# Kernel optimization log

Measured on AMD Instinct MI355X. Metric: run time of the kernel, lower is better.

## Reference

```python
import jax, jax.numpy as jnp
import numpy as np

HIDDEN = 2048
NUM_HEADS = 32
GROUP_SIZE = 4
HEAD_DIM = HIDDEN // NUM_HEADS            # 64
GROUP_NUM = NUM_HEADS // GROUP_SIZE       # 8 KV heads
B, S = 2, 2048


def setup_inputs() -> dict:
    key = jax.random.key(0)
    ks = jax.random.split(key, 7)
    sc = 1.0 / np.sqrt(HIDDEN)
    x = jax.random.normal(ks[0], (B, S, HIDDEN), dtype=jnp.float32)
    attention_mask = jnp.ones((B, S), dtype=jnp.int32)
    Wq = jax.random.normal(ks[1], (HIDDEN, HIDDEN), dtype=jnp.float32) * sc
    bq = jax.random.normal(ks[2], (HIDDEN,), dtype=jnp.float32) * 0.02
    Wk = jax.random.normal(ks[3], (HIDDEN, GROUP_NUM * HEAD_DIM), dtype=jnp.float32) * sc
    bk = jax.random.normal(ks[4], (GROUP_NUM * HEAD_DIM,), dtype=jnp.float32) * 0.02
    Wv = jax.random.normal(ks[5], (HIDDEN, GROUP_NUM * HEAD_DIM), dtype=jnp.float32) * sc
    bv = jax.random.normal(ks[6], (GROUP_NUM * HEAD_DIM,), dtype=jnp.float32) * 0.02
    return {"x": x, "attention_mask": attention_mask,
            "Wq": Wq, "bq": bq, "Wk": Wk, "bk": bk, "Wv": Wv, "bv": bv}


def reference(x, attention_mask, Wq, bq, Wk, bk, Wv, bv):
    b, s, _ = x.shape
    # projections
    q = (x @ Wq + bq).reshape(b, s, NUM_HEADS, HEAD_DIM).transpose(0, 2, 1, 3)   # (B,H,S,hd)
    k = (x @ Wk + bk).reshape(b, s, GROUP_NUM, HEAD_DIM).transpose(0, 2, 1, 3)   # (B,G,S,hd)
    v = (x @ Wv + bv).reshape(b, s, GROUP_NUM, HEAD_DIM).transpose(0, 2, 1, 3)
    # expand KV groups to full head count (head h uses group h // group_size)
    k = jnp.repeat(k, GROUP_SIZE, axis=1)                                        # (B,H,S,hd)
    v = jnp.repeat(v, GROUP_SIZE, axis=1)
    # NOTE: original torch code uses floor-division `//` for scaling and no softmax
    score = jnp.floor(jnp.einsum('bhqd,bhkd->bhqk', q, k) / np.sqrt(HEAD_DIM).astype(np.float32))
    score = jnp.where(attention_mask[:, None, None, :] == 0, -jnp.inf, score)
    out = jnp.einsum('bhqk,bhkd->bhqd', score, v)                                # (B,H,S,hd)
    return out.transpose(0, 2, 1, 3).reshape(b, s, HIDDEN)
```

## Files before the change

kernel.cpp:

```cpp
#include <hip/hip_runtime.h>
#include <math.h>

#define HIDDEN 2048
#define NHEADS 32
#define HDIM 64
#define GNUM 8
#define KVDIM 512
#define BB 2
#define SS 2048
#define MROWS (BB * SS)
#define NQKV 3072

typedef _Float16 half8 __attribute__((ext_vector_type(8)));
typedef _Float16 half4 __attribute__((ext_vector_type(4)));
typedef _Float16 half2 __attribute__((ext_vector_type(2)));
typedef __fp16 fp16x2 __attribute__((ext_vector_type(2)));
typedef float floatx4 __attribute__((ext_vector_type(4)));

#define MFMA16(a, b, c) __builtin_amdgcn_mfma_f32_16x16x32_f16((a), (b), (c), 0, 0, 0)

__device__ __forceinline__ void split_f32(float x, _Float16& hi, _Float16& lo) {
    hi = (_Float16)x;
    lo = (_Float16)((x - (float)hi) * 2048.0f);
}

__device__ __forceinline__ void load_lds16(const void* g, void* l) {
    __builtin_amdgcn_global_load_lds(
        (const __attribute__((address_space(1))) void*)g,
        (__attribute__((address_space(3))) void*)l, 16, 0, 0);
}

__device__ __forceinline__ void permswap32(unsigned& a, unsigned& b) {
    asm volatile("v_permlane32_swap_b32 %0, %1" : "+v"(a), "+v"(b));
}
__device__ __forceinline__ void permswap16(unsigned& a, unsigned& b) {
    asm volatile("v_permlane16_swap_b32 %0, %1" : "+v"(a), "+v"(b));
}

__device__ __forceinline__ unsigned pk_f16(float a, float b) {
    union { fp16x2 h; unsigned u; } c;
    c.h = __builtin_amdgcn_cvt_pkrtz(a, b);
    return c.u;
}

__global__ __launch_bounds__(256)
void split_x(const float* __restrict__ x, _Float16* __restrict__ xh,
             _Float16* __restrict__ xl, int n4) {
    for (int idx = blockIdx.x * 256 + threadIdx.x; idx < n4; idx += gridDim.x * 256) {
        floatx4 v = reinterpret_cast<const floatx4*>(x)[idx];
        half4 h, l;
        #pragma unroll
        for (int e = 0; e < 4; ++e) { _Float16 hi, lo; split_f32(v[e], hi, lo); h[e] = hi; l[e] = lo; }
        reinterpret_cast<half4*>(xh)[idx] = h;
        reinterpret_cast<half4*>(xl)[idx] = l;
    }
}

__global__ __launch_bounds__(256)
void split_wt(const float* __restrict__ W, int N, int n0,
              _Float16* __restrict__ Wth, _Float16* __restrict__ Wtl) {
    __shared__ float tile[64][68];
    const int tid = threadIdx.x;
    const int kb = blockIdx.x, nb = blockIdx.y;
    #pragma unroll
    for (int i = 0; i < 4; ++i) {
        int idx = tid + i * 256;
        int r = idx >> 4, c4 = idx & 15;
        floatx4 v = *reinterpret_cast<const floatx4*>(&W[(size_t)(kb * 64 + r) * N + nb * 64 + c4 * 4]);
        *reinterpret_cast<floatx4*>(&tile[r][c4 * 4]) = v;
    }
    __syncthreads();
    #pragma unroll
    for (int i = 0; i < 4; ++i) {
        int idx = tid + i * 256;
        int r2 = idx >> 4, c2 = (idx & 15) * 4;
        half4 h, l;
        #pragma unroll
        for (int e = 0; e < 4; ++e) {
            _Float16 hi, lo;
            split_f32(tile[c2 + e][r2], hi, lo);
            h[e] = hi; l[e] = lo;
        }
        size_t o = (size_t)(n0 + nb * 64 + r2) * HIDDEN + kb * 64 + c2;
        *reinterpret_cast<half4*>(&Wth[o]) = h;
        *reinterpret_cast<half4*>(&Wtl[o]) = l;
    }
}

__global__ __launch_bounds__(256)
void biascat_k(const float* __restrict__ bq, const float* __restrict__ bk,
               const float* __restrict__ bv, float* __restrict__ bias) {
    int i = blockIdx.x * 256 + threadIdx.x;
    if (i < 2048) bias[i] = bq[i];
    else if (i < 2560) bias[i] = bk[i - 2048];
    else if (i < NQKV) bias[i] = bv[i - 2560];
}

__global__ __launch_bounds__(256, 2)
void gemm_qkv(const _Float16* __restrict__ xh, const _Float16* __restrict__ xl,
              const _Float16* __restrict__ Wth, const _Float16* __restrict__ Wtl,
              const float* __restrict__ bias,
              _Float16* __restrict__ qh, _Float16* __restrict__ ql,
              _Float16* __restrict__ khs, _Float16* __restrict__ kls,
              _Float16* __restrict__ vh) {
    __shared__ __align__(16) _Float16 Ah[128 * 64];
    __shared__ __align__(16) _Float16 Al[128 * 64];
    __shared__ __align__(16) _Float16 Bh[128 * 64];
    __shared__ __align__(16) _Float16 Bl[128 * 64];

    const int tid  = threadIdx.x;
    const int lane = tid & 63;
    const int w    = tid >> 6;
    const int wm   = w >> 1, wn = w & 1;
    const int bm   = blockIdx.x, bn = blockIdx.y;
    const int ml   = lane & 15;
    const int kg8  = (lane >> 4) * 8;

    const _Float16* gsrc;
    _Float16* ldst;
    if      (w == 0) { gsrc = xh  + (size_t)(bm * 128) * HIDDEN; ldst = Ah; }
    else if (w == 1) { gsrc = xl  + (size_t)(bm * 128) * HIDDEN; ldst = Al; }
    else if (w == 2) { gsrc = Wth + (size_t)(bn * 128) * HIDDEN; ldst = Bh; }
    else             { gsrc = Wtl + (size_t)(bn * 128) * HIDDEN; ldst = Bl; }

    floatx4 acc0[4][4] = {};
    floatx4 accL[4][4] = {};

    for (int k0 = 0; k0 < HIDDEN; k0 += 64) {
        #pragma unroll
        for (int i = 0; i < 16; ++i) {
            int L   = i * 1024 + lane * 16;
            int row = L >> 7;
            int off = (L & 127) ^ ((row & 7) << 4);
            const void* gp = (const char*)(gsrc + (size_t)row * HIDDEN + k0) + off;
            void* lp = (char*)ldst + i * 1024;
            load_lds16(gp, lp);
        }
        __syncthreads();

        #pragma unroll
        for (int kc = 0; kc < 2; ++kc) {
            half8 a_h[4], a_l[4], b_h[4], b_l[4];
            #pragma unroll
            for (int r = 0; r < 4; ++r) {
                int row = wm * 64 + r * 16 + ml;
                int byt = row * 128 + (((kc * 64 + kg8 * 2)) ^ ((row & 7) << 4));
                a_h[r] = *reinterpret_cast<const half8*>((const char*)Ah + byt);
                a_l[r] = *reinterpret_cast<const half8*>((const char*)Al + byt);
            }
            #pragma unroll
            for (int c = 0; c < 4; ++c) {
                int row = wn * 64 + c * 16 + ml;
                int byt = row * 128 + (((kc * 64 + kg8 * 2)) ^ ((row & 7) << 4));
                b_h[c] = *reinterpret_cast<const half8*>((const char*)Bh + byt);
                b_l[c] = *reinterpret_cast<const half8*>((const char*)Bl + byt);
            }
            #pragma unroll
            for (int r = 0; r < 4; ++r)
                #pragma unroll
                for (int c = 0; c < 4; ++c) {
                    acc0[r][c] = MFMA16(a_h[r], b_h[c], acc0[r][c]);
                    accL[r][c] = MFMA16(a_h[r], b_l[c], accL[r][c]);
                    accL[r][c] = MFMA16(a_l[r], b_h[c], accL[r][c]);
                }
        }
        __syncthreads();
    }

    #pragma unroll
    for (int c = 0; c < 4; ++c) {
        int colg = bn * 128 + wn * 64 + c * 16 + ml;
        float bval = bias[colg];
        #pragma unroll
        for (int r = 0; r < 4; ++r) {
            int rowg = bm * 128 + wm * 64 + r * 16 + (lane >> 4) * 4;
            #pragma unroll
            for (int reg = 0; reg < 4; ++reg) {
                float val = acc0[r][c][reg] + accL[r][c][reg] * (1.0f / 2048.0f) + bval;
                int rr = rowg + reg;
                if (colg < 2048) {
                    _Float16 hi, lo; split_f32(val, hi, lo);
                    qh[(size_t)rr * HIDDEN + colg] = hi;
                    ql[(size_t)rr * HIDDEN + colg] = lo;
                } else if (colg < 2560) {
                    int ck = colg - 2048;
                    int gk = ck >> 6, dk = ck & 63;
                    int bk_ = rr >> 11, sk_ = rr & 2047;
                    int kk = sk_ & 63;
                    size_t baseK = ((size_t)((bk_ * 8 + gk) * 32 + (sk_ >> 6))) * 4096
                                 + kk * 64 + (dk ^ ((kk & 7) << 3));
                    _Float16 hi, lo; split_f32(val, hi, lo);
                    khs[baseK] = hi;
                    kls[baseK] = lo;
                } else {
                    vh[(size_t)rr * KVDIM + (colg - 2560)] = (_Float16)val;
                }
            }
        }
    }
}

__global__ __launch_bounds__(256, 2)
void attn5(const _Float16* __restrict__ qh, const _Float16* __restrict__ ql,
           const _Float16* __restrict__ khs, const _Float16* __restrict__ kls,
           const _Float16* __restrict__ vh, const int* __restrict__ mask,
           float* __restrict__ out) {
    __shared__ __align__(16) _Float16 Ksh[64 * 64];
    __shared__ __align__(16) _Float16 Ksl[64 * 64];
    __shared__ __align__(16) _Float16 Vst[64][72];

    const int tid  = threadIdx.x;
    const int lane = tid & 63;
    const int w    = tid >> 6;
    const int ml   = lane & 15;
    const int lg   = lane >> 4;
    const int kg8  = lg * 8;

    const int f_  = blockIdx.y * 32 + blockIdx.x;
    const int bg  = (f_ & 7) | ((f_ >> 8) << 3);
    const int qt  = (f_ >> 3) & 31;
    const int b   = bg >> 3, g = bg & 7;

    half8 qhf[4][2], qlf[4][2];
    {
        size_t rowbase = (size_t)(b * SS + qt * 64 + w * 16 + ml) * HIDDEN;
        #pragma unroll
        for (int hh = 0; hh < 4; ++hh) {
            int hcol = (g * 4 + hh) * HDIM;
            #pragma unroll
            for (int gch = 0; gch < 2; ++gch) {
                half8 a = *reinterpret_cast<const half8*>(&qh[rowbase + hcol + gch * 32 + kg8]);
                half8 c = *reinterpret_cast<const half8*>(&ql[rowbase + hcol + gch * 32 + kg8]);
                qhf[hh][gch] = a * (_Float16)0.125f;
                qlf[hh][gch] = c * (_Float16)0.125f;
            }
        }
    }

    const _Float16* ktile_h = khs + (size_t)(bg * 32) * 4096;
    const _Float16* ktile_l = kls + (size_t)(bg * 32) * 4096;
    const _Float16* vbg = vh + (size_t)b * SS * KVDIM + g * HDIM;
    const int* mb = mask + b * SS;

    floatx4 oacc[4][4] = {};

    for (int kt = 0; kt < SS / 64; ++kt) {
        __syncthreads();
        if (w == 0) {
            #pragma unroll
            for (int j = 0; j < 8; ++j)
                load_lds16((const char*)(ktile_h + (size_t)kt * 4096) + j * 1024 + lane * 16,
                           (char*)Ksh + j * 1024);
        } else if (w == 1) {
            #pragma unroll
            for (int j = 0; j < 8; ++j)
                load_lds16((const char*)(ktile_l + (size_t)kt * 4096) + j * 1024 + lane * 16,
                           (char*)Ksl + j * 1024);
        }
        {
            int rp = (tid & 31) * 2, c8 = (tid >> 5) * 8;
            half8 v0 = *reinterpret_cast<const half8*>(&vbg[(size_t)(kt * 64 + rp) * KVDIM + c8]);
            half8 v1 = *reinterpret_cast<const half8*>(&vbg[(size_t)(kt * 64 + rp + 1) * KVDIM + c8]);
            #pragma unroll
            for (int e = 0; e < 8; ++e)
                *reinterpret_cast<half2*>(&Vst[c8 + e][rp]) = half2{v0[e], v1[e]};
        }
        __syncthreads();

        half8 av[4][2];
        #pragma unroll
        for (int f = 0; f < 4; ++f)
            #pragma unroll
            for (int kc = 0; kc < 2; ++kc)
                av[f][kc] = *reinterpret_cast<const half8*>(&Vst[f * 16 + ml][kc * 32 + kg8]);

        int4 m4v[4];
        #pragma unroll
        for (int fc = 0; fc < 4; ++fc)
            m4v[fc] = *reinterpret_cast<const int4*>(&mb[kt * 64 + fc * 16 + lg * 4]);

        __builtin_amdgcn_s_setprio(1);

        unsigned h2[4][4][2];
        #pragma unroll
        for (int fc = 0; fc < 4; ++fc) {
            int krow = fc * 16 + ml;
            int xo = (krow & 7) << 3;
            half8 k_h[2], k_l[2];
            #pragma unroll
            for (int gch = 0; gch < 2; ++gch) {
                k_h[gch] = *reinterpret_cast<const half8*>(&Ksh[krow * 64 + ((gch * 32 + kg8) ^ xo)]);
                k_l[gch] = *reinterpret_cast<const half8*>(&Ksl[krow * 64 + ((gch * 32 + kg8) ^ xo)]);
            }
            #pragma unroll
            for (int hh = 0; hh < 4; ++hh) {
                floatx4 s0 = {}, sl = {};
                s0 = MFMA16(k_h[0], qhf[hh][0], s0);
                s0 = MFMA16(k_h[1], qhf[hh][1], s0);
                sl = MFMA16(k_l[0], qhf[hh][0], sl);
                sl = MFMA16(k_l[1], qhf[hh][1], sl);
                sl = MFMA16(k_h[0], qlf[hh][0], sl);
                sl = MFMA16(k_h[1], qlf[hh][1], sl);
                float sv[4];
                #pragma unroll
                for (int r = 0; r < 4; ++r) {
                    float t = floorf(fmaf(sl[r], 1.0f / 2048.0f, s0[r]));
                    sv[r] = (m4v[fc][r] == 0) ? -INFINITY : t;
                }
                h2[hh][fc][0] = pk_f16(sv[0], sv[1]);
                h2[hh][fc][1] = pk_f16(sv[2], sv[3]);
            }
        }

        #pragma unroll
        for (int hh = 0; hh < 4; ++hh) {
            #pragma unroll
            for (int kc = 0; kc < 2; ++kc) {
                unsigned t0 = h2[hh][2 * kc][0], tA = h2[hh][2 * kc + 1][0];
                unsigned t1 = h2[hh][2 * kc][1], tB = h2[hh][2 * kc + 1][1];
                permswap32(t0, tA); permswap16(t0, tA);
                permswap32(t1, tB); permswap16(t1, tB);
                union { unsigned u[4]; half8 h; } bu;
                bu.u[0] = t0; bu.u[1] = t1; bu.u[2] = tA; bu.u[3] = tB;
                #pragma unroll
                for (int f = 0; f < 4; ++f)
                    oacc[hh][f] = MFMA16(av[f][kc], bu.h, oacc[hh][f]);
            }
        }
        __builtin_amdgcn_s_setprio(0);
    }

    #pragma unroll
    for (int hh = 0; hh < 4; ++hh) {
        int hcol = (g * 4 + hh) * HDIM;
        #pragma unroll
        for (int f = 0; f < 4; ++f) {
            size_t row = (size_t)(b * SS + qt * 64 + w * 16 + ml);
            *reinterpret_cast<floatx4*>(&out[row * HIDDEN + hcol + f * 16 + lg * 4]) = oacc[hh][f];
        }
    }
}

extern "C" void kernel_launch(void* const* d_in, const int* in_sizes, int n_in,
                              void* d_out, int out_size, void* d_ws, size_t ws_size,
                              hipStream_t stream) {
    (void)in_sizes; (void)n_in; (void)out_size; (void)ws_size;
    const float* x    = (const float*)d_in[0];
    const int*   mask = (const int*)d_in[1];
    const float* Wq   = (const float*)d_in[2];
    const float* bq   = (const float*)d_in[3];
    const float* Wk   = (const float*)d_in[4];
    const float* bk   = (const float*)d_in[5];
    const float* Wv   = (const float*)d_in[6];
    const float* bv   = (const float*)d_in[7];

    _Float16* ws16 = (_Float16*)d_ws;
    size_t o = 0;
    auto alloc16 = [&](size_t n) { _Float16* p = ws16 + o; o += n; return p; };
    _Float16* xh  = alloc16((size_t)MROWS * HIDDEN);
    _Float16* xl  = alloc16((size_t)MROWS * HIDDEN);
    _Float16* Wth = alloc16((size_t)NQKV * HIDDEN);
    _Float16* Wtl = alloc16((size_t)NQKV * HIDDEN);
    _Float16* qh  = alloc16((size_t)MROWS * HIDDEN);
    _Float16* ql  = alloc16((size_t)MROWS * HIDDEN);
    _Float16* khs = alloc16((size_t)MROWS * KVDIM);
    _Float16* kls = alloc16((size_t)MROWS * KVDIM);
    _Float16* vh  = alloc16((size_t)MROWS * KVDIM);
    float* biascat = (float*)(ws16 + o);

    split_x<<<2048, 256, 0, stream>>>(x, xh, xl, MROWS * HIDDEN / 4);
    split_wt<<<dim3(32, 32), 256, 0, stream>>>(Wq, HIDDEN, 0,    Wth, Wtl);
    split_wt<<<dim3(32, 8),  256, 0, stream>>>(Wk, KVDIM, 2048, Wth, Wtl);
    split_wt<<<dim3(32, 8),  256, 0, stream>>>(Wv, KVDIM, 2560, Wth, Wtl);
    biascat_k<<<12, 256, 0, stream>>>(bq, bk, bv, biascat);
    gemm_qkv<<<dim3(MROWS / 128, NQKV / 128), 256, 0, stream>>>(
        xh, xl, Wth, Wtl, biascat, qh, ql, khs, kls, vh);
    attn5<<<dim3(32, 16), 256, 0, stream>>>(qh, ql, khs, kls, vh, mask, (float*)d_out);
}
```

Measured before the change: 305.6 us.

## Double-buffer QKV GEMM LDS tiles with K=32 stages and prefetch

Restructures the QKV projection GEMM main loop to use two LDS buffers of K=32 each, issuing async global-to-LDS loads for the next tile while the current tile is consumed by MFMAs. It uses explicit vmcnt waits and barriers, adjusts the XOR swizzle for the 64-byte rows, and raises wave priority around the MFMA block. Total LDS stays the same. The goal is to hide global load latency behind compute, at the cost of twice as many barriers per unit of K and smaller per-iteration work.

```diff
diff --git a/kernel.cpp b/kernel.cpp
--- a/kernel.cpp
+++ b/kernel.cpp
@@ -103,10 +103,10 @@
               _Float16* __restrict__ qh, _Float16* __restrict__ ql,
               _Float16* __restrict__ khs, _Float16* __restrict__ kls,
               _Float16* __restrict__ vh) {
-    __shared__ __align__(16) _Float16 Ah[128 * 64];
-    __shared__ __align__(16) _Float16 Al[128 * 64];
-    __shared__ __align__(16) _Float16 Bh[128 * 64];
-    __shared__ __align__(16) _Float16 Bl[128 * 64];
+    __shared__ __align__(16) _Float16 Ah[2][128 * 32];
+    __shared__ __align__(16) _Float16 Al[2][128 * 32];
+    __shared__ __align__(16) _Float16 Bh[2][128 * 32];
+    __shared__ __align__(16) _Float16 Bl[2][128 * 32];
 
     const int tid  = threadIdx.x;
     const int lane = tid & 63;
@@ -117,54 +117,69 @@
     const int kg8  = (lane >> 4) * 8;
 
     const _Float16* gsrc;
-    _Float16* ldst;
-    if      (w == 0) { gsrc = xh  + (size_t)(bm * 128) * HIDDEN; ldst = Ah; }
-    else if (w == 1) { gsrc = xl  + (size_t)(bm * 128) * HIDDEN; ldst = Al; }
-    else if (w == 2) { gsrc = Wth + (size_t)(bn * 128) * HIDDEN; ldst = Bh; }
-    else             { gsrc = Wtl + (size_t)(bn * 128) * HIDDEN; ldst = Bl; }
+    char* ldst;
+    if      (w == 0) { gsrc = xh  + (size_t)(bm * 128) * HIDDEN; ldst = (char*)&Ah[0][0]; }
+    else if (w == 1) { gsrc = xl  + (size_t)(bm * 128) * HIDDEN; ldst = (char*)&Al[0][0]; }
+    else if (w == 2) { gsrc = Wth + (size_t)(bn * 128) * HIDDEN; ldst = (char*)&Bh[0][0]; }
+    else             { gsrc = Wtl + (size_t)(bn * 128) * HIDDEN; ldst = (char*)&Bl[0][0]; }
+
+    auto stage = [&](int d, int k0) {
+        #pragma unroll
+        for (int i = 0; i < 8; ++i) {
+            int L   = i * 1024 + lane * 16;
+            int row = L >> 6;
+            int off = (L & 63) ^ (((row >> 1) & 3) << 4);
+            load_lds16((const char*)(gsrc + (size_t)row * HIDDEN + k0) + off,
+                       ldst + d * 8192 + i * 1024);
+        }
+    };
 
     floatx4 acc0[4][4] = {};
     floatx4 accL[4][4] = {};
 
-    for (int k0 = 0; k0 < HIDDEN; k0 += 64) {
-        #pragma unroll
-        for (int i = 0; i < 16; ++i) {
-            int L   = i * 1024 + lane * 16;
-            int row = L >> 7;
-            int off = (L & 127) ^ ((row & 7) << 4);
-            const void* gp = (const char*)(gsrc + (size_t)row * HIDDEN + k0) + off;
-            void* lp = (char*)ldst + i * 1024;
-            load_lds16(gp, lp);
-        }
-        __syncthreads();
-
-        #pragma unroll
-        for (int kc = 0; kc < 2; ++kc) {
-            half8 a_h[4], a_l[4], b_h[4], b_l[4];
-            #pragma unroll
-            for (int r = 0; r < 4; ++r) {
-                int row = wm * 64 + r * 16 + ml;
-                int byt = row * 128 + (((kc * 64 + kg8 * 2)) ^ ((row & 7) << 4));
-                a_h[r] = *reinterpret_cast<const half8*>((const char*)Ah + byt);
-                a_l[r] = *reinterpret_cast<const half8*>((const char*)Al + byt);
-            }
+    const int NT = HIDDEN / 32;
+    stage(0, 0);
+
+    for (int t = 0; t < NT; ++t) {
+        const int cur = t & 1;
+        __builtin_amdgcn_sched_barrier(0);
+        __builtin_amdgcn_s_barrier();
+        __builtin_amdgcn_sched_barrier(0);
+        if (t + 1 < NT) {
+            stage(cur ^ 1, (t + 1) * 32);
+            asm volatile("s_waitcnt vmcnt(8)" ::: "memory");
+        } else {
+            asm volatile("s_waitcnt vmcnt(0)" ::: "memory");
+        }
+        __builtin_amdgcn_sched_barrier(0);
+        __builtin_amdgcn_s_barrier();
+        __builtin_amdgcn_sched_barrier(0);
+
+        half8 a_h[4], a_l[4], b_h[4], b_l[4];
+        #pragma unroll
+        for (int r = 0; r < 4; ++r) {
+            int row = wm * 64 + r * 16 + ml;
+            int byt = cur * 8192 + row * 64 + ((kg8 * 2) ^ (((row >> 1) & 3) << 4));
+            a_h[r] = *reinterpret_cast<const half8*>((const char*)Ah + byt);
+            a_l[r] = *reinterpret_cast<const half8*>((const char*)Al + byt);
+        }
+        #pragma unroll
+        for (int c = 0; c < 4; ++c) {
+            int row = wn * 64 + c * 16 + ml;
+            int byt = cur * 8192 + row * 64 + ((kg8 * 2) ^ (((row >> 1) & 3) << 4));
+            b_h[c] = *reinterpret_cast<const half8*>((const char*)Bh + byt);
+            b_l[c] = *reinterpret_cast<const half8*>((const char*)Bl + byt);
+        }
+        __builtin_amdgcn_s_setprio(1);
+        #pragma unroll
+        for (int r = 0; r < 4; ++r)
             #pragma unroll
             for (int c = 0; c < 4; ++c) {
-                int row = wn * 64 + c * 16 + ml;
-                int byt = row * 128 + (((kc * 64 + kg8 * 2)) ^ ((row & 7) << 4));
-                b_h[c] = *reinterpret_cast<const half8*>((const char*)Bh + byt);
-                b_l[c] = *reinterpret_cast<const half8*>((const char*)Bl + byt);
-            }
-            #pragma unroll
-            for (int r = 0; r < 4; ++r)
-                #pragma unroll
-                for (int c = 0; c < 4; ++c) {
-                    acc0[r][c] = MFMA16(a_h[r], b_h[c], acc0[r][c]);
-                    accL[r][c] = MFMA16(a_h[r], b_l[c], accL[r][c]);
-                    accL[r][c] = MFMA16(a_l[r], b_h[c], accL[r][c]);
-                }
-        }
-        __syncthreads();
+                acc0[r][c] = MFMA16(a_h[r], b_h[c], acc0[r][c]);
+                accL[r][c] = MFMA16(a_h[r], b_l[c], accL[r][c]);
+                accL[r][c] = MFMA16(a_l[r], b_h[c], accL[r][c]);
+            }
+        __builtin_amdgcn_s_setprio(0);
     }
 
     #pragma unroll
```

Result: no change. 306.3 us (+0.2%).
